# Performance work log

Measured on AMD Instinct MI355X. Metric: run time of the kernel, lower is better.

Reference implementation:

```python
import jax, jax.numpy as jnp
import numpy as np

N = 50000   # nodes
E = 800000  # edges (before self-loops)
IN, HID, OUT = 128, 128, 64


def gcn_norm(edge_index, num_nodes):
    # add self loops with weight 1, then symmetric deg^-1/2 normalization
    loop = jnp.arange(num_nodes, dtype=edge_index.dtype)
    row = jnp.concatenate([edge_index[0], loop])
    col = jnp.concatenate([edge_index[1], loop])
    ew = jnp.ones(row.shape[0], dtype=jnp.float32)
    deg = jax.ops.segment_sum(ew, col, num_segments=num_nodes)
    dis = jnp.where(deg > 0, jax.lax.rsqrt(deg), 0.0)
    norm = dis[row] * ew * dis[col]
    return row, col, norm


def gcn_conv(x, row, col, norm, W, b):
    h = x @ W                                   # [N, F_out] dense GEMM
    msg = h[row] * norm[:, None]                # gather + scale over edges
    out = jax.ops.segment_sum(msg, col, num_segments=x.shape[0])  # scatter-add
    return out + b


def setup_inputs() -> dict:
    key = jax.random.key(0)
    k0, k1, k2, k3, k4, k5 = jax.random.split(key, 6)
    x = jax.random.normal(k0, (N, IN), dtype=jnp.float32)
    edge_index = jax.random.randint(k1, (2, E), 0, N, dtype=jnp.int32)
    # glorot-style init for linear weights, zeros for bias (PyG default)
    W1 = jax.random.normal(k2, (IN, HID), dtype=jnp.float32) * np.float32(np.sqrt(1.0 / IN))
    b1 = jnp.zeros((HID,), dtype=jnp.float32)
    W2 = jax.random.normal(k3, (HID, OUT), dtype=jnp.float32) * np.float32(np.sqrt(1.0 / HID))
    b2 = jnp.zeros((OUT,), dtype=jnp.float32)
    return {"x": x, "edge_index": edge_index, "W1": W1, "b1": b1, "W2": W2, "b2": b2}


def reference(x, edge_index, W1, b1, W2, b2):
    row, col, norm = gcn_norm(edge_index, x.shape[0])
    h = jax.nn.relu(gcn_conv(x, row, col, norm, W1, b1))
    # dropout is a no-op in eval mode (training=False)
    out = gcn_conv(h, row, col, norm, W2, b2)
    return out
```

## Files before the change

### kernel.cpp

```cpp
#include <hip/hip_runtime.h>
#include <hip/hip_fp16.h>


#define Nn 50000
#define Ne 800000
#define NE2 (Ne / 2)
#define SCAN_B ((Nn + 1023) / 1024)
#define GT32 ((Nn + 31) / 32)
#define E1B ((NE2 + 255) / 256)
#define READY (1 << 30)

using f16x8 = _Float16 __attribute__((ext_vector_type(8)));
using f32x4 = float __attribute__((ext_vector_type(4)));

__global__ __launch_bounds__(256) void k_prep(const float* __restrict__ W1,
                                              const float* __restrict__ W2,
                                              _Float16* __restrict__ W1h,
                                              _Float16* __restrict__ W2h,
                                              int* __restrict__ degi,
                                              int* __restrict__ bstate) {
  const int b = blockIdx.x, t = threadIdx.x;
  if (b < 49) {
    int i = b * 256 + t;
    if (i < Nn / 4) ((int4*)degi)[i] = make_int4(0, 0, 0, 0);
    if (b == 0 && t < 64) bstate[t] = 0;
  } else if (b == 49) {
    for (int i = 0; i < 8; ++i) {
      int id = i * 256 + t;
      int c = id & 127, k8 = id >> 7;
      f16x8 hv;
      #pragma unroll
      for (int j = 0; j < 8; ++j) hv[j] = (_Float16)W1[(k8 * 8 + j) * 128 + c];
      *(f16x8*)&W1h[c * 128 + ((k8 ^ (c & 7)) << 3)] = hv;
    }
  } else {
    for (int i = 0; i < 4; ++i) {
      int id = i * 256 + t;
      int c = id & 63, k8 = id >> 6;
      f16x8 hv;
      #pragma unroll
      for (int j = 0; j < 8; ++j) hv[j] = (_Float16)W2[(k8 * 8 + j) * 64 + c];
      *(f16x8*)&W2h[c * 128 + ((k8 ^ (c & 7)) << 3)] = hv;
    }
  }
}

__global__ __launch_bounds__(256, 5) void k_gemm32_count(
    const float* __restrict__ X, const _Float16* __restrict__ W1h,
    __half* __restrict__ H, const int2* __restrict__ col2,
    int* __restrict__ degi, ushort2* __restrict__ rank2) {
  __shared__ _Float16 Wts[128 * 128];
  _Float16* Hsx = Wts;

  const int tid = threadIdx.x;
  const int base = blockIdx.x * 32;

  {
    const f16x8* src = (const f16x8*)W1h;
    f16x8* dst = (f16x8*)Wts;
    #pragma unroll
    for (int i = 0; i < 8; ++i) dst[i * 256 + tid] = src[i * 256 + tid];
  }

  {
    int i0 = blockIdx.x * 256 + tid;
    if (i0 < NE2) {
      int2 c = col2[i0];
      ushort2 rk;
      rk.x = (unsigned short)atomicAdd(&degi[c.x], 1);
      rk.y = (unsigned short)atomicAdd(&degi[c.y], 1);
      rank2[i0] = rk;
    }
  }

  const int w = tid >> 6, lane = tid & 63;
  const int quad = lane >> 4, mrow = lane & 15;
  const int rbase = (w & 1) * 16, cbase = (w >> 1) * 64;
  int anode = base + rbase + mrow;
  if (anode >= Nn) anode = Nn - 1;
  const float4* xg = (const float4*)(X + (size_t)anode * 128);
  f16x8 av[4];
  #pragma unroll
  for (int ko = 0; ko < 4; ++ko) {
    float4 x0 = xg[ko * 8 + quad * 2];
    float4 x1 = xg[ko * 8 + quad * 2 + 1];
    av[ko][0] = (_Float16)x0.x; av[ko][1] = (_Float16)x0.y;
    av[ko][2] = (_Float16)x0.z; av[ko][3] = (_Float16)x0.w;
    av[ko][4] = (_Float16)x1.x; av[ko][5] = (_Float16)x1.y;
    av[ko][6] = (_Float16)x1.z; av[ko][7] = (_Float16)x1.w;
  }
  __syncthreads();

  f32x4 acc[4];
  #pragma unroll
  for (int ct = 0; ct < 4; ++ct) acc[ct] = (f32x4){0.f, 0.f, 0.f, 0.f};

  #pragma unroll
  for (int ko = 0; ko < 4; ++ko) {
    #pragma unroll
    for (int ct = 0; ct < 4; ++ct) {
      int c = cbase + ct * 16 + mrow;
      f16x8 bv = *(const f16x8*)&Wts[c * 128 + (((ko * 4 + quad) ^ (c & 7)) << 3)];
      acc[ct] = __builtin_amdgcn_mfma_f32_16x16x32_f16(av[ko], bv, acc[ct], 0, 0, 0);
    }
  }

  __syncthreads();
  #pragma unroll
  for (int ct = 0; ct < 4; ++ct) {
    #pragma unroll
    for (int r = 0; r < 4; ++r)
      Hsx[(rbase + quad * 4 + r) * 136 + cbase + ct * 16 + mrow] =
          (_Float16)acc[ct][r];
  }
  __syncthreads();

  #pragma unroll
  for (int i = 0; i < 2; ++i) {
    int id = i * 256 + tid;
    int r = id >> 4, ch = id & 15;
    int node = base + r;
    if (node < Nn)
      *(f16x8*)((_Float16*)H + (size_t)node * 128 + ch * 8) =
          *(const f16x8*)&Hsx[r * 136 + ch * 8];
  }
}

__global__ __launch_bounds__(1024) void k_scan_lb(const int* __restrict__ degi,
                                                  int* __restrict__ rowptr,
                                                  float* __restrict__ dis,
                                                  int* __restrict__ bstate) {
  __shared__ int wsum[16];
  __shared__ int off_s;
  const int tid = threadIdx.x;
  const int bid = blockIdx.x;
  const int lane = tid & 63, wid = tid >> 6;
  const int i = bid * 1024 + tid;

  int v = (i < Nn) ? degi[i] : 0;
  if (i < Nn) dis[i] = rsqrtf((float)(v + 1));
  int incl = v;
  #pragma unroll
  for (int off = 1; off < 64; off <<= 1) {
    int t = __shfl_up(incl, off);
    if (lane >= off) incl += t;
  }
  if (lane == 63) wsum[wid] = incl;
  __syncthreads();
  if (wid == 0) {
    int wv = (lane < 16) ? wsum[lane] : 0;
    #pragma unroll
    for (int off = 1; off < 16; off <<= 1) {
      int t = __shfl_up(wv, off);
      if (lane >= off) wv += t;
    }
    if (lane < 16) wsum[lane] = wv;
    if (lane == 15) atomicExch(&bstate[bid], wv | READY);
  }
  __syncthreads();
  if (wid == 0) {
    int sum = 0;
    if (lane < bid) {
      int bv;
      do { bv = atomicAdd(&bstate[lane], 0); } while (!(bv & READY));
      sum = bv & ~READY;
    }
    #pragma unroll
    for (int off = 32; off >= 1; off >>= 1) sum += __shfl_xor(sum, off);
    if (lane == 0) off_s = sum;
  }
  __syncthreads();
  int woff = (wid > 0) ? wsum[wid - 1] : 0;
  if (i <= Nn) rowptr[i] = off_s + woff + incl - v;
}

__global__ __launch_bounds__(256) void k_fill(const int2* __restrict__ row2,
                                              const int2* __restrict__ col2,
                                              const int* __restrict__ rowptr,
                                              const ushort2* __restrict__ rank2,
                                              unsigned short* __restrict__ csr) {
  int t = blockIdx.x * 256 + threadIdx.x;
  if (t >= NE2) return;
  int2 r = row2[t];
  int2 c = col2[t];
  ushort2 k = rank2[t];
  csr[rowptr[c.x] + (int)k.x] = (unsigned short)r.x;
  csr[rowptr[c.y] + (int)k.y] = (unsigned short)r.y;
}

__device__ __forceinline__ float2 h2f(unsigned int u) {
  return __half22float2(*(const __half2*)&u);
}

__global__ __launch_bounds__(256) void k_agg128_gemm64(
    const __half* __restrict__ H, const unsigned short* __restrict__ csr,
    const int* __restrict__ rowptr, const float* __restrict__ dis,
    const float* __restrict__ bias, const _Float16* __restrict__ W2h,
    __half* __restrict__ H2, int n) {
  __shared__ _Float16 Wts[64 * 128];
  __shared__ _Float16 Hs[16 * 136];

  const int tid = threadIdx.x;
  const int wid = tid >> 6, lane = tid & 63;
  const int sub = lane >> 4, fl = lane & 15;
  const int nb = wid * 4 + sub;
  const int v = blockIdx.x * 16 + nb;

  {
    const f16x8* src = (const f16x8*)W2h;
    f16x8* dst = (f16x8*)Wts;
    #pragma unroll
    for (int i = 0; i < 4; ++i) dst[i * 256 + tid] = src[i * 256 + tid];
  }

  int s = rowptr[v], e = rowptr[v + 1];
  float d = dis[v];
  float sw = d * d;
  const uint4* Hq = (const uint4*)H;
  uint4 hv = Hq[(size_t)v * 16 + fl];
  float2 p0 = h2f(hv.x), p1 = h2f(hv.y), p2 = h2f(hv.z), p3 = h2f(hv.w);
  float a0 = p0.x * sw, a1 = p0.y * sw, a2 = p1.x * sw, a3 = p1.y * sw;
  float a4 = p2.x * sw, a5 = p2.y * sw, a6 = p3.x * sw, a7 = p3.y * sw;
  constexpr int D = 6;
  if (s < e) {
    int srcs[D];
    #pragma unroll
    for (int j = 0; j < D; ++j) {
      int idx = s + j;
      srcs[j] = csr[(idx < e) ? idx : (e - 1)];
    }
    int base = s;
    for (; base + D <= e; base += D) {
      uint4 q[D];
      float wd[D];
      #pragma unroll
      for (int j = 0; j < D; ++j) q[j] = Hq[(size_t)srcs[j] * 16 + fl];
      #pragma unroll
      for (int j = 0; j < D; ++j) wd[j] = dis[srcs[j]];
      int ns[D];
      #pragma unroll
      for (int j = 0; j < D; ++j) {
        int idx = base + D + j;
        ns[j] = csr[(idx < e) ? idx : (e - 1)];
      }
      #pragma unroll
      for (int j = 0; j < D; ++j) {
        float w = wd[j] * d;
        float2 t;
        t = h2f(q[j].x); a0 = fmaf(w, t.x, a0); a1 = fmaf(w, t.y, a1);
        t = h2f(q[j].y); a2 = fmaf(w, t.x, a2); a3 = fmaf(w, t.y, a3);
        t = h2f(q[j].z); a4 = fmaf(w, t.x, a4); a5 = fmaf(w, t.y, a5);
        t = h2f(q[j].w); a6 = fmaf(w, t.x, a6); a7 = fmaf(w, t.y, a7);
      }
      #pragma unroll
      for (int j = 0; j < D; ++j) srcs[j] = ns[j];
    }
    if (base < e) {
      uint4 q[D];
      float wd[D];
      #pragma unroll
      for (int j = 0; j < D; ++j) q[j] = Hq[(size_t)srcs[j] * 16 + fl];
      #pragma unroll
      for (int j = 0; j < D; ++j) wd[j] = dis[srcs[j]];
      #pragma unroll
      for (int j = 0; j < D; ++j) {
        float w = (base + j < e) ? wd[j] * d : 0.f;
        float2 t;
        t = h2f(q[j].x); a0 = fmaf(w, t.x, a0); a1 = fmaf(w, t.y, a1);
        t = h2f(q[j].y); a2 = fmaf(w, t.x, a2); a3 = fmaf(w, t.y, a3);
        t = h2f(q[j].z); a4 = fmaf(w, t.x, a4); a5 = fmaf(w, t.y, a5);
        t = h2f(q[j].w); a6 = fmaf(w, t.x, a6); a7 = fmaf(w, t.y, a7);
      }
    }
  }
  {
    const float4* Bq = (const float4*)bias;
    float4 b0 = Bq[fl * 2], b1v = Bq[fl * 2 + 1];
    f16x8 hrow;
    hrow[0] = (_Float16)fmaxf(a0 + b0.x, 0.f);
    hrow[1] = (_Float16)fmaxf(a1 + b0.y, 0.f);
    hrow[2] = (_Float16)fmaxf(a2 + b0.z, 0.f);
    hrow[3] = (_Float16)fmaxf(a3 + b0.w, 0.f);
    hrow[4] = (_Float16)fmaxf(a4 + b1v.x, 0.f);
    hrow[5] = (_Float16)fmaxf(a5 + b1v.y, 0.f);
    hrow[6] = (_Float16)fmaxf(a6 + b1v.z, 0.f);
    hrow[7] = (_Float16)fmaxf(a7 + b1v.w, 0.f);
    *(f16x8*)&Hs[nb * 136 + fl * 8] = hrow;
  }
  __syncthreads();

  const int quad = lane >> 4, mrow = lane & 15;
  f32x4 acc = (f32x4){0.f, 0.f, 0.f, 0.f};
  const int c = wid * 16 + mrow;
  #pragma unroll
  for (int ko = 0; ko < 4; ++ko) {
    f16x8 avx = *(const f16x8*)&Hs[mrow * 136 + ko * 32 + quad * 8];
    f16x8 bv = *(const f16x8*)&Wts[c * 128 + (((ko * 4 + quad) ^ (c & 7)) << 3)];
    acc = __builtin_amdgcn_mfma_f32_16x16x32_f16(avx, bv, acc, 0, 0, 0);
  }

  __syncthreads();
  #pragma unroll
  for (int r = 0; r < 4; ++r)
    Hs[(quad * 4 + r) * 136 + wid * 16 + mrow] = (_Float16)acc[r];
  __syncthreads();

  if (tid < 128) {
    int r = tid >> 3, ch = tid & 7;
    *(f16x8*)((_Float16*)H2 + ((size_t)blockIdx.x * 16 + r) * 64 + ch * 8) =
        *(const f16x8*)&Hs[r * 136 + ch * 8];
  }
}

__global__ __launch_bounds__(256) void k_agg64(const __half* __restrict__ H,
                                               const unsigned short* __restrict__ csr,
                                               const int* __restrict__ rowptr,
                                               const float* __restrict__ dis,
                                               const float* __restrict__ bias,
                                               float* __restrict__ Out, int n) {
  const int wid = threadIdx.x >> 6, lane = threadIdx.x & 63;
  const int sub = lane >> 4, fl = lane & 15;
  int v = blockIdx.x * 16 + wid * 4 + sub;
  if (v >= n) return;
  int s = rowptr[v], e = rowptr[v + 1];
  float d = dis[v];
  float sw = d * d;
  const uint2* Hq = (const uint2*)H;
  uint2 hv = Hq[(size_t)v * 16 + fl];
  float2 p0 = h2f(hv.x), p1 = h2f(hv.y);
  float a0 = p0.x * sw, a1 = p0.y * sw, a2 = p1.x * sw, a3 = p1.y * sw;
  constexpr int D = 8;
  if (s < e) {
    int srcs[D];
    #pragma unroll
    for (int j = 0; j < D; ++j) {
      int idx = s + j;
      srcs[j] = csr[(idx < e) ? idx : (e - 1)];
    }
    int base = s;
    for (; base + D <= e; base += D) {
      uint2 q[D];
      float wd[D];
      #pragma unroll
      for (int j = 0; j < D; ++j) q[j] = Hq[(size_t)srcs[j] * 16 + fl];
      #pragma unroll
      for (int j = 0; j < D; ++j) wd[j] = dis[srcs[j]];
      int ns[D];
      #pragma unroll
      for (int j = 0; j < D; ++j) {
        int idx = base + D + j;
        ns[j] = csr[(idx < e) ? idx : (e - 1)];
      }
      #pragma unroll
      for (int j = 0; j < D; ++j) {
        float w = wd[j] * d;
        float2 t;
        t = h2f(q[j].x); a0 = fmaf(w, t.x, a0); a1 = fmaf(w, t.y, a1);
        t = h2f(q[j].y); a2 = fmaf(w, t.x, a2); a3 = fmaf(w, t.y, a3);
      }
      #pragma unroll
      for (int j = 0; j < D; ++j) srcs[j] = ns[j];
    }
    if (base < e) {
      uint2 q[D];
      float wd[D];
      #pragma unroll
      for (int j = 0; j < D; ++j) q[j] = Hq[(size_t)srcs[j] * 16 + fl];
      #pragma unroll
      for (int j = 0; j < D; ++j) wd[j] = dis[srcs[j]];
      #pragma unroll
      for (int j = 0; j < D; ++j) {
        float w = (base + j < e) ? wd[j] * d : 0.f;
        float2 t;
        t = h2f(q[j].x); a0 = fmaf(w, t.x, a0); a1 = fmaf(w, t.y, a1);
        t = h2f(q[j].y); a2 = fmaf(w, t.x, a2); a3 = fmaf(w, t.y, a3);
      }
    }
  }
  const float4* Bq = (const float4*)bias;
  float4 b = Bq[fl];
  float4 o = make_float4(a0 + b.x, a1 + b.y, a2 + b.z, a3 + b.w);
  ((float4*)(Out + (size_t)v * 64))[fl] = o;
}

extern "C" void kernel_launch(void* const* d_in, const int* in_sizes, int n_in,
                              void* d_out, int out_size, void* d_ws, size_t ws_size,
                              hipStream_t stream) {
  const float* x  = (const float*)d_in[0];
  const int*   ei = (const int*)d_in[1];
  const int*   row = ei;
  const int*   col = ei + Ne;
  const float* W1 = (const float*)d_in[2];
  const float* b1 = (const float*)d_in[3];
  const float* W2 = (const float*)d_in[4];
  const float* b2 = (const float*)d_in[5];
  float* out = (float*)d_out;

  char* ws = (char*)d_ws;
  size_t off = 0;
  auto alloc = [&](size_t bytes) -> void* {
    void* p = ws + off;
    off += (bytes + 255) & ~(size_t)255;
    return p;
  };
  int*    degi   = (int*)   alloc(Nn * sizeof(int));
  int*    rowptr = (int*)   alloc((Nn + 1) * sizeof(int));
  float*  dis    = (float*) alloc(Nn * sizeof(float));
  int*    bstate = (int*)   alloc(64 * sizeof(int));
  unsigned short* rank = (unsigned short*)alloc((size_t)Ne * sizeof(unsigned short));
  unsigned short* csr  = (unsigned short*)alloc((size_t)Ne * sizeof(unsigned short));
  __half* H1     = (__half*)alloc((size_t)Nn * 128 * sizeof(__half));
  __half* H2     = (__half*)alloc((size_t)Nn * 64 * sizeof(__half));
  _Float16* W1h  = (_Float16*)alloc(128 * 128 * sizeof(_Float16));
  _Float16* W2h  = (_Float16*)alloc(64 * 128 * sizeof(_Float16));

  const int NGB = (Nn + 15) / 16;

  k_prep<<<51, 256, 0, stream>>>(W1, W2, W1h, W2h, degi, bstate);
  k_gemm32_count<<<GT32, 256, 0, stream>>>(x, W1h, H1, (const int2*)col,
                                           degi, (ushort2*)rank);
  k_scan_lb<<<SCAN_B, 1024, 0, stream>>>(degi, rowptr, dis, bstate);
  k_fill<<<E1B, 256, 0, stream>>>((const int2*)row, (const int2*)col, rowptr,
                                  (const ushort2*)rank, csr);
  k_agg128_gemm64<<<NGB, 256, 0, stream>>>(H1, csr, rowptr, dis, b1, W2h, H2, Nn);
  k_agg64<<<NGB, 256, 0, stream>>>(H2, csr, rowptr, dis, b2, out, Nn);
}
```

Baseline: 182.2 us.

## Fuse weight prep into GEMM and merge scan with CSR fill

Removes the separate prep kernel. Every GEMM block now converts W1 to swizzled fp16 in shared memory itself, block 0 writes W2h, and a memset replaces the degree/state zeroing. The scan and CSR fill kernels merge into one launch with a device-wide completion counter and spin-wait, so two launches and their gaps disappear. In exchange, every GEMM block re-reads and converts W1 from fp32. The fused kernel also depends on all scan blocks being resident or scheduled before the fill blocks spin, which risks deadlock or stalls.

```diff
diff --git a/kernel.cpp b/kernel.cpp
--- a/kernel.cpp
+++ b/kernel.cpp
@@ -5,61 +5,34 @@
 #define Nn 50000
 #define Ne 800000
 #define NE2 (Ne / 2)
-#define SCAN_B ((Nn + 1023) / 1024)
 #define GT32 ((Nn + 31) / 32)
 #define E1B ((NE2 + 255) / 256)
+#define SB  ((Nn + 255) / 256)
+#define DONE_IDX 200
 #define READY (1 << 30)
 
 using f16x8 = _Float16 __attribute__((ext_vector_type(8)));
 using f32x4 = float __attribute__((ext_vector_type(4)));
 
-__global__ __launch_bounds__(256) void k_prep(const float* __restrict__ W1,
-                                              const float* __restrict__ W2,
-                                              _Float16* __restrict__ W1h,
-                                              _Float16* __restrict__ W2h,
-                                              int* __restrict__ degi,
-                                              int* __restrict__ bstate) {
-  const int b = blockIdx.x, t = threadIdx.x;
-  if (b < 49) {
-    int i = b * 256 + t;
-    if (i < Nn / 4) ((int4*)degi)[i] = make_int4(0, 0, 0, 0);
-    if (b == 0 && t < 64) bstate[t] = 0;
-  } else if (b == 49) {
-    for (int i = 0; i < 8; ++i) {
-      int id = i * 256 + t;
-      int c = id & 127, k8 = id >> 7;
-      f16x8 hv;
-      #pragma unroll
-      for (int j = 0; j < 8; ++j) hv[j] = (_Float16)W1[(k8 * 8 + j) * 128 + c];
-      *(f16x8*)&W1h[c * 128 + ((k8 ^ (c & 7)) << 3)] = hv;
-    }
-  } else {
-    for (int i = 0; i < 4; ++i) {
-      int id = i * 256 + t;
-      int c = id & 63, k8 = id >> 6;
-      f16x8 hv;
-      #pragma unroll
-      for (int j = 0; j < 8; ++j) hv[j] = (_Float16)W2[(k8 * 8 + j) * 64 + c];
-      *(f16x8*)&W2h[c * 128 + ((k8 ^ (c & 7)) << 3)] = hv;
-    }
-  }
-}
-
 __global__ __launch_bounds__(256, 5) void k_gemm32_count(
-    const float* __restrict__ X, const _Float16* __restrict__ W1h,
-    __half* __restrict__ H, const int2* __restrict__ col2,
-    int* __restrict__ degi, ushort2* __restrict__ rank2) {
+    const float* __restrict__ X, const float* __restrict__ W1,
+    const float* __restrict__ W2, __half* __restrict__ H,
+    const int2* __restrict__ col2, int* __restrict__ degi,
+    ushort2* __restrict__ rank2, _Float16* __restrict__ W2h) {
   __shared__ _Float16 Wts[128 * 128];
   _Float16* Hsx = Wts;
 
   const int tid = threadIdx.x;
   const int base = blockIdx.x * 32;
 
-  {
-    const f16x8* src = (const f16x8*)W1h;
-    f16x8* dst = (f16x8*)Wts;
-    #pragma unroll
-    for (int i = 0; i < 8; ++i) dst[i * 256 + tid] = src[i * 256 + tid];
+  #pragma unroll
+  for (int i = 0; i < 8; ++i) {
+    int idx = i * 256 + tid;
+    int k8 = idx & 15, c = idx >> 4;
+    f16x8 hv;
+    #pragma unroll
+    for (int j = 0; j < 8; ++j) hv[j] = (_Float16)W1[(k8 * 8 + j) * 128 + c];
+    *(f16x8*)&Wts[c * 128 + ((k8 ^ (c & 7)) << 3)] = hv;
   }
 
   {
@@ -73,6 +46,18 @@
     }
   }
 
+  if (blockIdx.x == 0) {
+    #pragma unroll
+    for (int i = 0; i < 4; ++i) {
+      int idx = i * 256 + tid;
+      int k8 = idx & 15, c = idx >> 4;
+      f16x8 hv;
+      #pragma unroll
+      for (int j = 0; j < 8; ++j) hv[j] = (_Float16)W2[(k8 * 8 + j) * 64 + c];
+      *(f16x8*)&W2h[c * 128 + ((k8 ^ (c & 7)) << 3)] = hv;
+    }
+  }
+
   const int w = tid >> 6, lane = tid & 63;
   const int quad = lane >> 4, mrow = lane & 15;
   const int rbase = (w & 1) * 16, cbase = (w >> 1) * 64;
@@ -126,66 +111,73 @@
   }
 }
 
-__global__ __launch_bounds__(1024) void k_scan_lb(const int* __restrict__ degi,
-                                                  int* __restrict__ rowptr,
-                                                  float* __restrict__ dis,
-                                                  int* __restrict__ bstate) {
-  __shared__ int wsum[16];
+__global__ __launch_bounds__(256) void k_scanfill(
+    const int* __restrict__ degi, int* __restrict__ rowptr,
+    float* __restrict__ dis, int* __restrict__ bstate,
+    const int2* __restrict__ row2, const int2* __restrict__ col2,
+    const ushort2* __restrict__ rank2, unsigned short* __restrict__ csr) {
+  __shared__ int wsum[4];
   __shared__ int off_s;
-  const int tid = threadIdx.x;
-  const int bid = blockIdx.x;
+  const int tid = threadIdx.x, bid = blockIdx.x;
   const int lane = tid & 63, wid = tid >> 6;
-  const int i = bid * 1024 + tid;
-
-  int v = (i < Nn) ? degi[i] : 0;
-  if (i < Nn) dis[i] = rsqrtf((float)(v + 1));
-  int incl = v;
-  #pragma unroll
-  for (int off = 1; off < 64; off <<= 1) {
-    int t = __shfl_up(incl, off);
-    if (lane >= off) incl += t;
-  }
-  if (lane == 63) wsum[wid] = incl;
-  __syncthreads();
-  if (wid == 0) {
-    int wv = (lane < 16) ? wsum[lane] : 0;
-    #pragma unroll
-    for (int off = 1; off < 16; off <<= 1) {
-      int t = __shfl_up(wv, off);
-      if (lane >= off) wv += t;
-    }
-    if (lane < 16) wsum[lane] = wv;
-    if (lane == 15) atomicExch(&bstate[bid], wv | READY);
-  }
-  __syncthreads();
-  if (wid == 0) {
-    int sum = 0;
-    if (lane < bid) {
-      int bv;
-      do { bv = atomicAdd(&bstate[lane], 0); } while (!(bv & READY));
-      sum = bv & ~READY;
-    }
-    #pragma unroll
-    for (int off = 32; off >= 1; off >>= 1) sum += __shfl_xor(sum, off);
-    if (lane == 0) off_s = sum;
-  }
-  __syncthreads();
-  int woff = (wid > 0) ? wsum[wid - 1] : 0;
-  if (i <= Nn) rowptr[i] = off_s + woff + incl - v;
-}
-
-__global__ __launch_bounds__(256) void k_fill(const int2* __restrict__ row2,
-                                              const int2* __restrict__ col2,
-                                              const int* __restrict__ rowptr,
-                                              const ushort2* __restrict__ rank2,
-                                              unsigned short* __restrict__ csr) {
-  int t = blockIdx.x * 256 + threadIdx.x;
-  if (t >= NE2) return;
-  int2 r = row2[t];
-  int2 c = col2[t];
-  ushort2 k = rank2[t];
-  csr[rowptr[c.x] + (int)k.x] = (unsigned short)r.x;
-  csr[rowptr[c.y] + (int)k.y] = (unsigned short)r.y;
+
+  if (bid < SB) {
+    const int i = bid * 256 + tid;
+    int v = (i < Nn) ? degi[i] : 0;
+    if (i < Nn) dis[i] = rsqrtf((float)(v + 1));
+    int incl = v;
+    #pragma unroll
+    for (int off = 1; off < 64; off <<= 1) {
+      int t = __shfl_up(incl, off);
+      if (lane >= off) incl += t;
+    }
+    if (lane == 63) wsum[wid] = incl;
+    __syncthreads();
+    if (tid == 0) {
+      int a = wsum[0], b = wsum[1], c = wsum[2], d = wsum[3];
+      wsum[0] = 0; wsum[1] = a; wsum[2] = a + b; wsum[3] = a + b + c;
+      atomicExch(&bstate[bid], (a + b + c + d) | READY);
+    }
+    __syncthreads();
+    if (wid == 0) {
+      int sum = 0;
+      for (int j = lane; j < bid; j += 64) {
+        int bv;
+        do { bv = atomicAdd(&bstate[j], 0); } while (!(bv & READY));
+        sum += bv & ~READY;
+      }
+      #pragma unroll
+      for (int off = 32; off >= 1; off >>= 1) sum += __shfl_xor(sum, off);
+      if (lane == 0) off_s = sum;
+    }
+    __syncthreads();
+    int g = off_s + wsum[wid] + incl - v;
+    if (i < Nn) rowptr[i] = g;
+    if (i == Nn - 1) rowptr[Nn] = g + v;
+    __syncthreads();
+    if (tid == 0) {
+      __threadfence();
+      atomicAdd(&bstate[DONE_IDX], 1);
+    }
+  }
+
+  if (tid == 0) {
+    while (atomicAdd(&bstate[DONE_IDX], 0) < SB) __builtin_amdgcn_s_sleep(16);
+  }
+  __syncthreads();
+
+  int t = bid * 256 + tid;
+  if (t < NE2) {
+    int2 r = row2[t];
+    int2 c = col2[t];
+    ushort2 k = rank2[t];
+    int p0 = __hip_atomic_load(&rowptr[c.x], __ATOMIC_RELAXED,
+                               __HIP_MEMORY_SCOPE_AGENT);
+    int p1 = __hip_atomic_load(&rowptr[c.y], __ATOMIC_RELAXED,
+                               __HIP_MEMORY_SCOPE_AGENT);
+    csr[p0 + (int)k.x] = (unsigned short)r.x;
+    csr[p1 + (int)k.y] = (unsigned short)r.y;
+  }
 }
 
 __device__ __forceinline__ float2 h2f(unsigned int u) {
@@ -404,24 +396,24 @@
     return p;
   };
   int*    degi   = (int*)   alloc(Nn * sizeof(int));
+  int*    bstate = (int*)   alloc(256 * sizeof(int));
   int*    rowptr = (int*)   alloc((Nn + 1) * sizeof(int));
   float*  dis    = (float*) alloc(Nn * sizeof(float));
-  int*    bstate = (int*)   alloc(64 * sizeof(int));
   unsigned short* rank = (unsigned short*)alloc((size_t)Ne * sizeof(unsigned short));
   unsigned short* csr  = (unsigned short*)alloc((size_t)Ne * sizeof(unsigned short));
   __half* H1     = (__half*)alloc((size_t)Nn * 128 * sizeof(__half));
   __half* H2     = (__half*)alloc((size_t)Nn * 64 * sizeof(__half));
-  _Float16* W1h  = (_Float16*)alloc(128 * 128 * sizeof(_Float16));
   _Float16* W2h  = (_Float16*)alloc(64 * 128 * sizeof(_Float16));
 
   const int NGB = (Nn + 15) / 16;
 
-  k_prep<<<51, 256, 0, stream>>>(W1, W2, W1h, W2h, degi, bstate);
-  k_gemm32_count<<<GT32, 256, 0, stream>>>(x, W1h, H1, (const int2*)col,
-                                           degi, (ushort2*)rank);
-  k_scan_lb<<<SCAN_B, 1024, 0, stream>>>(degi, rowptr, dis, bstate);
-  k_fill<<<E1B, 256, 0, stream>>>((const int2*)row, (const int2*)col, rowptr,
-                                  (const ushort2*)rank, csr);
+  hipMemsetAsync(degi, 0, ((Nn * sizeof(int) + 255) & ~(size_t)255)
+                              + 256 * sizeof(int), stream);
+  k_gemm32_count<<<GT32, 256, 0, stream>>>(x, W1, W2, H1, (const int2*)col,
+                                           degi, (ushort2*)rank, W2h);
+  k_scanfill<<<E1B, 256, 0, stream>>>(degi, rowptr, dis, bstate,
+                                      (const int2*)row, (const int2*)col,
+                                      (const ushort2*)rank, csr);
   k_agg128_gemm64<<<NGB, 256, 0, stream>>>(H1, csr, rowptr, dis, b1, W2h, H2, Nn);
   k_agg64<<<NGB, 256, 0, stream>>>(H2, csr, rowptr, dis, b2, out, Nn);
 }
```

New measurement: 240.5 us. 32.0% more time.
